# Performance work log

Measured on AMD Instinct MI355X. Metric: run time of the kernel, lower is better.

## Reference

```python
import jax, jax.numpy as jnp
import numpy as np

B, S, H, E, V, L = 64, 400, 512, 300, 50000, 1


def setup_inputs() -> dict:
    key = jax.random.key(0)
    ks = jax.random.split(key, 16)
    s = lambda k, shape, fan: jax.random.normal(k, shape, jnp.float32) * (1.0 / np.sqrt(fan))
    return {
        "x": jax.random.randint(ks[0], (B,), 0, V),
        "enc_out": jax.random.normal(ks[1], (B, S, H), jnp.float32),
        "h0": jax.random.normal(ks[2], (L, B, H), jnp.float32),
        "c0": jax.random.normal(ks[3], (L, B, H), jnp.float32),
        "text": jax.random.randint(ks[4], (B, S), 0, V),
        "batch_size": B,
        "emb_table": jax.random.normal(ks[5], (V, E), jnp.float32),
        "V_w": s(ks[6], (1, H), H),
        "V_b": jnp.zeros((1,), jnp.float32),
        "gen_w": s(ks[7], (1, 2 * H + E), 2 * H + E),
        "gen_b": jnp.zeros((1,), jnp.float32),
        "out_w": s(ks[8], (V, 2 * H), 2 * H),
        "out_b": jnp.zeros((V,), jnp.float32),
        "W_ih": s(ks[9], (4 * H, E + H), E + H),
        "W_hh": s(ks[10], (4 * H, H), H),
        "b_ih": jnp.zeros((4 * H,), jnp.float32),
        "b_hh": jnp.zeros((4 * H,), jnp.float32),
    }


def reference(x, enc_out, h0, c0, text, batch_size, emb_table, V_w, V_b,
              gen_w, gen_b, out_w, out_b, W_ih, W_hh, b_ih, b_hh):
    xe = emb_table[x]                                   # [B,E] (dropout off in eval)
    h_prev, c_prev = h0[0], c0[0]                       # [B,H], layers==1
    # Bahdanau attention: V(tanh(enc_out + dec_h)) softmaxed over seq
    score = jnp.tanh(enc_out + h_prev[:, None, :]) @ V_w.T + V_b   # [B,S,1]
    enc_weight = jax.nn.softmax(score, axis=1)                      # [B,S,1]
    ctx = jnp.sum(enc_weight * enc_out, axis=1)                     # [B,H]
    # single-step LSTM cell (torch gate order: i,f,g,o)
    d_in = jnp.concatenate([xe, ctx], axis=-1)                      # [B,E+H]
    gates = d_in @ W_ih.T + h_prev @ W_hh.T + b_ih + b_hh           # [B,4H]
    i, f, g, o = jnp.split(gates, 4, axis=-1)
    c_new = jax.nn.sigmoid(f) * c_prev + jax.nn.sigmoid(i) * jnp.tanh(g)
    h_new = jax.nn.sigmoid(o) * jnp.tanh(c_new)                     # [B,H]
    # pointer-generator combine
    out_cat = jnp.concatenate([h_new, ctx], axis=-1)                # [B,2H]
    gen_in = jnp.concatenate([ctx, h_new, xe], axis=-1)             # [B,2H+E]
    p_gen = jax.nn.sigmoid(gen_in @ gen_w.T + gen_b)[:, 0]          # [B]
    p_ptr = 1.0 - p_gen
    rows = jnp.arange(batch_size)[:, None]                          # [B,1]
    ptr_prob = jnp.zeros((batch_size, out_w.shape[0]), enc_out.dtype)
    ptr_prob = ptr_prob.at[rows, text].set(enc_weight[:, :, 0])     # scatter-set
    gen_prob = out_cat @ out_w.T + out_b                            # [B,V]
    out_prob = p_ptr[:, None] * ptr_prob + p_gen[:, None] * gen_prob
    return out_prob, h_new[None], c_new[None]
```

## Files before the change

kernel.cpp:

```cpp
#include <hip/hip_runtime.h>
#include <hip/hip_bf16.h>

#define BB 64
#define SS 400
#define HH 512
#define EE 300
#define VV 50000
#define KD 812
#define KG 1324
#define KC 1024
#define BV (BB*VV)

typedef __attribute__((ext_vector_type(8))) short bf16x8;
typedef __attribute__((ext_vector_type(4))) float f32x4;
typedef __attribute__((address_space(1))) const void gv_t;
typedef __attribute__((address_space(3))) void lv_t;

#define WS_SCORE 0
#define WS_W     25600
#define WS_CTX   51200
#define WS_HNEW  83968
#define WS_G0    116736
#define WS_G1    247808
#define WS_G2    378880
#define WS_G3    509952
#define WS_PGEN  641024
#define WS_PART  641088
#define WS_ABF   903232
#define WS_AD1   936000
#define WS_AD2   962624

__device__ __forceinline__ float sigm(float x){ return 1.f/(1.f+__expf(-x)); }
__device__ __forceinline__ float ftanh(float x){
  x = fminf(fmaxf(x,-15.f),15.f);
  float e = __expf(2.f*x);
  return (e-1.f)/(e+1.f);
}
__device__ __forceinline__ unsigned short f2bf(float f){
  unsigned int u = __builtin_bit_cast(unsigned int, f);
  u += 0x7fffu + ((u>>16)&1u);
  return (unsigned short)(u>>16);
}

#define LDW(S, off) { w##S##0 = *(const float4*)(wr + (off)*32); \
                      w##S##1 = *(const float4*)(wr + (off)*32 + 4); }
#define LDA(S, off) { a##S##0 = *(const bf16x8*)(a0 + (off)*32); \
                      a##S##1 = *(const bf16x8*)(a1 + (off)*32); \
                      a##S##2 = *(const bf16x8*)(a2 + (off)*32); \
                      a##S##3 = *(const bf16x8*)(a3 + (off)*32); }
#define CONS(S) { union { bf16x8 v; unsigned int u[4]; } bb_; \
  float4 f0_ = w##S##0; float4 f1_ = w##S##1; \
  asm("v_cvt_pk_bf16_f32 %0, %1, %2" : "=v"(bb_.u[0]) : "v"(f0_.x), "v"(f0_.y)); \
  asm("v_cvt_pk_bf16_f32 %0, %1, %2" : "=v"(bb_.u[1]) : "v"(f0_.z), "v"(f0_.w)); \
  asm("v_cvt_pk_bf16_f32 %0, %1, %2" : "=v"(bb_.u[2]) : "v"(f1_.x), "v"(f1_.y)); \
  asm("v_cvt_pk_bf16_f32 %0, %1, %2" : "=v"(bb_.u[3]) : "v"(f1_.z), "v"(f1_.w)); \
  acc0 = __builtin_amdgcn_mfma_f32_16x16x32_bf16(a##S##0, bb_.v, acc0, 0,0,0); \
  acc1 = __builtin_amdgcn_mfma_f32_16x16x32_bf16(a##S##1, bb_.v, acc1, 0,0,0); \
  acc2 = __builtin_amdgcn_mfma_f32_16x16x32_bf16(a##S##2, bb_.v, acc2, 0,0,0); \
  acc3 = __builtin_amdgcn_mfma_f32_16x16x32_bf16(a##S##3, bb_.v, acc3, 0,0,0); }

template<int NSTEP>
__device__ __forceinline__ void mfma_seg2(const float* __restrict__ wr,
    const unsigned short* __restrict__ a0, const unsigned short* __restrict__ a1,
    const unsigned short* __restrict__ a2, const unsigned short* __restrict__ a3,
    f32x4& acc0, f32x4& acc1, f32x4& acc2, f32x4& acc3)
{
  static_assert(NSTEP % 2 == 0 && NSTEP >= 4, "");
  float4 wA0,wA1, wB0,wB1;
  bf16x8 aA0,aA1,aA2,aA3, aB0,aB1,aB2,aB3;
  LDW(A,0) LDA(A,0)
  LDW(B,1) LDA(B,1)
  #pragma unroll
  for (int ks=0; ks<NSTEP; ks+=2){
    CONS(A) if (ks+2 < NSTEP){ LDW(A,ks+2) LDA(A,ks+2) }
    CONS(B) if (ks+3 < NSTEP){ LDW(B,ks+3) LDA(B,ks+3) }
  }
}

__global__ __launch_bounds__(256) void k_prep(const int* __restrict__ x,
    const float* __restrict__ emb, const float* __restrict__ h0,
    unsigned short* __restrict__ ad1, unsigned short* __restrict__ ad2)
{
  int n = blockIdx.x*256 + threadIdx.x;
  if (n < BB*832){
    int b = n/832, k = n - b*832;
    if (k < EE) ad1[n] = f2bf(emb[(size_t)x[b]*EE + k]);
    else if (k >= 812) ad1[n] = 0;
  } else {
    int m = n - BB*832;
    ad2[m] = f2bf(h0[m]);
  }
}

__global__ __launch_bounds__(256) void k_score(const float* __restrict__ enc,
    const float* __restrict__ h0, const float* __restrict__ Vw,
    const float* __restrict__ Vb, float* __restrict__ score)
{
  int wv = threadIdx.x >> 6, lane = threadIdx.x & 63;
  int pair = blockIdx.x*4 + wv;
  int b = pair / SS;
  int i0 = lane*8;
  const float4* ep = (const float4*)(enc + (size_t)pair*HH + i0);
  const float4* hp = (const float4*)(h0 + b*HH + i0);
  const float4* vp = (const float4*)(Vw + i0);
  float4 e0 = ep[0], e1 = ep[1];
  float4 hv0 = hp[0], hv1 = hp[1];
  float4 v0 = vp[0], v1 = vp[1];
  float sum = ftanh(e0.x+hv0.x)*v0.x + ftanh(e0.y+hv0.y)*v0.y
            + ftanh(e0.z+hv0.z)*v0.z + ftanh(e0.w+hv0.w)*v0.w
            + ftanh(e1.x+hv1.x)*v1.x + ftanh(e1.y+hv1.y)*v1.y
            + ftanh(e1.z+hv1.z)*v1.z + ftanh(e1.w+hv1.w)*v1.w;
  #pragma unroll
  for (int off=32; off; off>>=1) sum += __shfl_xor(sum, off);
  if (lane==0) score[pair] = sum + Vb[0];
}

__global__ __launch_bounds__(256) void k_ctx(const float* __restrict__ enc,
    const float* __restrict__ score, float* __restrict__ wout,
    float* __restrict__ part)
{
  __shared__ float red[256];
  __shared__ float wl[SS];
  int b = blockIdx.x >> 3, sp = blockIdx.x & 7;
  int t = threadIdx.x;
  float v1 = score[b*SS + t];
  float v2 = (t < SS-256) ? score[b*SS + t + 256] : -1e30f;
  red[t] = fmaxf(v1, v2);
  __syncthreads();
  for (int o=128; o; o>>=1){ if (t<o) red[t] = fmaxf(red[t], red[t+o]); __syncthreads(); }
  float mx = red[0];
  __syncthreads();
  float e1 = __expf(v1 - mx);
  float e2 = (t < SS-256) ? __expf(v2 - mx) : 0.f;
  red[t] = e1 + e2;
  __syncthreads();
  for (int o=128; o; o>>=1){ if (t<o) red[t] += red[t+o]; __syncthreads(); }
  float inv = 1.f/red[0];
  float w1 = e1*inv;
  wl[t] = w1;
  if (sp==0) wout[b*SS + t] = w1;
  if (t < SS-256){
    float w2 = e2*inv;
    wl[t+256] = w2;
    if (sp==0) wout[b*SS + t + 256] = w2;
  }
  __syncthreads();
  float a0 = 0.f, a1 = 0.f;
  const float* ebase = enc + ((size_t)b*SS + sp*50)*HH + 2*t;
  #pragma unroll 5
  for (int s=0; s<50; ++s){
    float wg = wl[sp*50 + s];
    float2 e = *(const float2*)(ebase + s*HH);
    a0 += wg * e.x;
    a1 += wg * e.y;
  }
  *(float2*)(part + (size_t)(b*8+sp)*HH + 2*t) = make_float2(a0, a1);
}

__global__ __launch_bounds__(256) void k_ctx_reduce(const float* __restrict__ part,
    float* __restrict__ ctx, unsigned short* __restrict__ ad1)
{
  int b = blockIdx.x, t = threadIdx.x;
  float a0=0.f, a1=0.f;
  #pragma unroll
  for (int sp=0; sp<8; ++sp){
    float2 e = *(const float2*)(part + (size_t)(b*8+sp)*HH + 2*t);
    a0 += e.x; a1 += e.y;
  }
  *(float2*)(ctx + b*HH + 2*t) = make_float2(a0, a1);
  ad1[b*832 + EE + 2*t]     = f2bf(a0);
  ad1[b*832 + EE + 2*t + 1] = f2bf(a1);
}

__global__ __launch_bounds__(128, 4) void k_gates(const float* __restrict__ Wih,
    const float* __restrict__ Whh, const unsigned short* __restrict__ ad1,
    const unsigned short* __restrict__ ad2,
    float* __restrict__ g0, float* __restrict__ g1,
    float* __restrict__ g2, float* __restrict__ g3)
{
  int wt = blockIdx.x*2 + (threadIdx.x >> 6);
  int lane = threadIdx.x & 63;
  int col = lane & 15, kg = lane >> 4;
  int jt = wt >> 2, part = wt & 3;
  int j = jt*16 + col;
  f32x4 acc0={0.f,0.f,0.f,0.f}, acc1=acc0, acc2=acc0, acc3=acc0;
  float* g;
  if (part < 2){
    int k0 = part ? 384 : 0;
    const float* wr = Wih + (size_t)j*KD + k0 + kg*8;
    const unsigned short* a = ad1 + col*832 + k0 + kg*8;
    if (part) mfma_seg2<14>(wr, a, a+16*832, a+32*832, a+48*832, acc0,acc1,acc2,acc3);
    else      mfma_seg2<12>(wr, a, a+16*832, a+32*832, a+48*832, acc0,acc1,acc2,acc3);
    g = part ? g1 : g0;
  } else {
    int k0 = (part==3) ? 256 : 0;
    const float* wr = Whh + (size_t)j*HH + k0 + kg*8;
    const unsigned short* a = ad2 + col*512 + k0 + kg*8;
    mfma_seg2<8>(wr, a, a+16*512, a+32*512, a+48*512, acc0,acc1,acc2,acc3);
    g = (part==3) ? g3 : g2;
  }
  #pragma unroll
  for (int i=0;i<4;i++){
    g[(size_t)j*BB + 0*16 + kg*4 + i] = acc0[i];
    g[(size_t)j*BB + 1*16 + kg*4 + i] = acc1[i];
    g[(size_t)j*BB + 2*16 + kg*4 + i] = acc2[i];
    g[(size_t)j*BB + 3*16 + kg*4 + i] = acc3[i];
  }
}

__global__ __launch_bounds__(256) void k_lstm(const float* __restrict__ c0,
    const float* __restrict__ bih, const float* __restrict__ bhh,
    const float* __restrict__ g0, const float* __restrict__ g1,
    const float* __restrict__ g2, const float* __restrict__ g3,
    const float* __restrict__ ctx, float* __restrict__ hnew,
    unsigned short* __restrict__ abf, float* __restrict__ out)
{
  int n = blockIdx.x*256 + threadIdx.x;
  int b = n & 63, h = n >> 6;
  #define GSUM(off) (g0[(off)*BB+b] + g1[(off)*BB+b] + g2[(off)*BB+b] + g3[(off)*BB+b] + bih[off] + bhh[off])
  float gi = GSUM(h);
  float gf = GSUM(HH+h);
  float gg = GSUM(2*HH+h);
  float go = GSUM(3*HH+h);
  #undef GSUM
  float cn = sigm(gf)*c0[b*HH+h] + sigm(gi)*ftanh(gg);
  float hn = sigm(go)*ftanh(cn);
  out[BV + b*HH + h]          = hn;
  out[BV + BB*HH + b*HH + h]  = cn;
  hnew[b*HH + h] = hn;
  abf[b*KC + h]      = f2bf(hn);
  abf[b*KC + HH + h] = f2bf(ctx[b*HH + h]);
}

__global__ __launch_bounds__(256) void k_pgen(const float* __restrict__ genw,
    const float* __restrict__ genb, const float* __restrict__ ctx,
    const float* __restrict__ hnew, const int* __restrict__ x,
    const float* __restrict__ emb, float* __restrict__ pgen)
{
  __shared__ float red[256];
  int b = blockIdx.x, t = threadIdx.x;
  float p = 0.f;
  for (int k=t; k<KG; k+=256){
    float g = genw[k];
    float v = (k < HH) ? ctx[b*HH + k]
            : (k < 2*HH) ? hnew[b*HH + k - HH]
            : emb[(size_t)x[b]*EE + (k - 2*HH)];
    p += g*v;
  }
  red[t] = p; __syncthreads();
  for (int o=128; o; o>>=1){ if (t<o) red[t] += red[t+o]; __syncthreads(); }
  if (t==0) pgen[b] = sigm(red[0] + genb[0]);
}

#define ROWB 4096
#define HROWB 2048
#define PADH 2064
__global__ __launch_bounds__(256, 2) void k_gemm(const float* __restrict__ out_w,
    const float* __restrict__ out_b, const unsigned short* __restrict__ abf,
    const float* __restrict__ pgen, float* __restrict__ out)
{
  __shared__ __align__(16) char wlds[2][16*PADH];
  int t = threadIdx.x;
  int w = t >> 6, lane = t & 63;
  int col = lane & 15, kg = lane >> 4;
  int bid = blockIdx.x;
  int ts = (bid * 3125) >> 9;
  int te = ((bid + 1) * 3125) >> 9;

  const unsigned short* ap = abf + (size_t)(w*16 + col)*KC + kg*8;
  bf16x8 pa0[16], pa1[16];
  #pragma unroll
  for (int ks=0; ks<16; ++ks){
    pa0[ks] = *(const bf16x8*)(ap + ks*32);
    pa1[ks] = *(const bf16x8*)(ap + 512 + ks*32);
  }

  #define DMASTEP(buf_, tile_, kh_) { \
    const char* wb_ = (const char*)out_w + (size_t)(tile_)*16*ROWB + (kh_)*HROWB; \
    _Pragma("unroll") \
    for (int i_=0;i_<8;i_++){ \
      int c_ = w*8 + i_; \
      int r_ = c_ >> 1, q_ = c_ & 1; \
      __builtin_amdgcn_global_load_lds( \
        (gv_t*)(wb_ + (size_t)r_*ROWB + q_*1024 + lane*16), \
        (lv_t*)(&wlds[buf_][0] + r_*PADH + q_*1024), 16, 0, 0); \
    } }

  #define HALFCOMPUTE(buf_, PA_) { \
    const char* rb_ = &wlds[buf_][0] + col*PADH + kg*32; \
    _Pragma("unroll") \
    for (int ks=0; ks<16; ++ks){ \
      float4 f0 = *(const float4*)(rb_ + ks*128); \
      float4 f1 = *(const float4*)(rb_ + ks*128 + 16); \
      union { bf16x8 v; unsigned int u[4]; } bb; \
      asm("v_cvt_pk_bf16_f32 %0, %1, %2" : "=v"(bb.u[0]) : "v"(f0.x), "v"(f0.y)); \
      asm("v_cvt_pk_bf16_f32 %0, %1, %2" : "=v"(bb.u[1]) : "v"(f0.z), "v"(f0.w)); \
      asm("v_cvt_pk_bf16_f32 %0, %1, %2" : "=v"(bb.u[2]) : "v"(f1.x), "v"(f1.y)); \
      asm("v_cvt_pk_bf16_f32 %0, %1, %2" : "=v"(bb.u[3]) : "v"(f1.z), "v"(f1.w)); \
      acc = __builtin_amdgcn_mfma_f32_16x16x32_bf16(PA_[ks], bb.v, acc, 0,0,0); \
    } }

  DMASTEP(0, ts, 0)
  int cur = 0;
  for (int tile = ts; tile < te; ++tile){
    f32x4 acc = {0.f,0.f,0.f,0.f};

    __syncthreads();
    DMASTEP(cur^1, tile, 1)
    HALFCOMPUTE(cur, pa0)
    cur ^= 1;

    __syncthreads();
    if (tile + 1 < te) DMASTEP(cur^1, tile+1, 0)
    HALFCOMPUTE(cur, pa1)
    cur ^= 1;

    int v = tile*16 + col;
    float ob = out_b[v];
    #pragma unroll
    for (int i=0;i<4;i++){
      int b = w*16 + kg*4 + i;
      out[(size_t)b*VV + v] = pgen[b]*(acc[i] + ob);
    }
  }
  #undef DMASTEP
  #undef HALFCOMPUTE
}

__global__ __launch_bounds__(256) void k_scatter(const int* __restrict__ text,
    const float* __restrict__ w, const float* __restrict__ pgen,
    float* __restrict__ out)
{
  __shared__ int ts[SS];
  int b = blockIdx.x, t = threadIdx.x;
  ts[t] = text[b*SS + t];
  if (t + 256 < SS) ts[t+256] = text[b*SS + t + 256];
  __syncthreads();
  float pp = 1.f - pgen[b];
  #pragma unroll
  for (int rep=0; rep<2; ++rep){
    int s = t + rep*256;
    if (s < SS){
      int v = ts[s];
      bool dup = false;
      #pragma unroll 4
      for (int s2=s+1; s2<SS; ++s2) dup = dup || (ts[s2]==v);
      if (!dup) out[(size_t)b*VV + v] += pp * w[b*SS + s];
    }
  }
}

extern "C" void kernel_launch(void* const* d_in, const int* in_sizes, int n_in,
                              void* d_out, int out_size, void* d_ws, size_t ws_size,
                              hipStream_t stream)
{
  const int*   x    = (const int*)  d_in[0];
  const float* enc  = (const float*)d_in[1];
  const float* h0   = (const float*)d_in[2];
  const float* c0   = (const float*)d_in[3];
  const int*   text = (const int*)  d_in[4];
  const float* emb  = (const float*)d_in[6];
  const float* Vw   = (const float*)d_in[7];
  const float* Vb   = (const float*)d_in[8];
  const float* genw = (const float*)d_in[9];
  const float* genb = (const float*)d_in[10];
  const float* outw = (const float*)d_in[11];
  const float* outb = (const float*)d_in[12];
  const float* Wih  = (const float*)d_in[13];
  const float* Whh  = (const float*)d_in[14];
  const float* bih  = (const float*)d_in[15];
  const float* bhh  = (const float*)d_in[16];
  float* out = (float*)d_out;

  float* ws     = (float*)d_ws;
  float* score  = ws + WS_SCORE;
  float* wbuf   = ws + WS_W;
  float* ctx    = ws + WS_CTX;
  float* hnew   = ws + WS_HNEW;
  float* g0     = ws + WS_G0;
  float* g1     = ws + WS_G1;
  float* g2     = ws + WS_G2;
  float* g3     = ws + WS_G3;
  float* pgen   = ws + WS_PGEN;
  float* part   = ws + WS_PART;
  unsigned short* abf = (unsigned short*)(ws + WS_ABF);
  unsigned short* ad1 = (unsigned short*)(ws + WS_AD1);
  unsigned short* ad2 = (unsigned short*)(ws + WS_AD2);

  k_prep<<<336, 256, 0, stream>>>(x, emb, h0, ad1, ad2);
  k_score<<<6400, 256, 0, stream>>>(enc, h0, Vw, Vb, score);
  k_ctx<<<512, 256, 0, stream>>>(enc, score, wbuf, part);
  k_ctx_reduce<<<64, 256, 0, stream>>>(part, ctx, ad1);
  k_gates<<<256, 128, 0, stream>>>(Wih, Whh, ad1, ad2, g0, g1, g2, g3);
  k_lstm<<<128, 256, 0, stream>>>(c0, bih, bhh, g0, g1, g2, g3, ctx, hnew, abf, out);
  k_pgen<<<64, 256, 0, stream>>>(genw, genb, ctx, hnew, x, emb, pgen);
  k_gemm<<<512, 256, 0, stream>>>(outw, outb, abf, pgen, out);
  k_scatter<<<64, 256, 0, stream>>>(text, wbuf, pgen, out);
}
```

Measured before the change: 126.1 us.

## Fuse score into ctx with split softmax; restage gemm weight loads via registers

The score and context kernels merge into one. Each block scores its own 50-position chunk, keeps a local max and sum, and writes unnormalised partial contexts that the reduce kernel rescales flash-style. The scatter kernel recomputes the normalised weights from the scores. Separately, the output GEMM drops direct global-to-LDS DMA in favour of register-staged quarter-K double buffering with manual waitcnt and barriers. This removes a launch and a second pass over enc_out, at the cost of different load scheduling and more barriers in the GEMM.

```diff
diff --git a/kernel.cpp b/kernel.cpp
--- a/kernel.cpp
+++ b/kernel.cpp
@@ -13,11 +13,10 @@
 
 typedef __attribute__((ext_vector_type(8))) short bf16x8;
 typedef __attribute__((ext_vector_type(4))) float f32x4;
-typedef __attribute__((address_space(1))) const void gv_t;
-typedef __attribute__((address_space(3))) void lv_t;
 
 #define WS_SCORE 0
-#define WS_W     25600
+#define WS_ML    25600
+#define WS_MLB   26624
 #define WS_CTX   51200
 #define WS_HNEW  83968
 #define WS_G0    116736
@@ -92,84 +91,79 @@
   }
 }
 
-__global__ __launch_bounds__(256) void k_score(const float* __restrict__ enc,
+__global__ __launch_bounds__(256) void k_scorectx(const float* __restrict__ enc,
     const float* __restrict__ h0, const float* __restrict__ Vw,
-    const float* __restrict__ Vb, float* __restrict__ score)
-{
-  int wv = threadIdx.x >> 6, lane = threadIdx.x & 63;
-  int pair = blockIdx.x*4 + wv;
-  int b = pair / SS;
+    const float* __restrict__ Vb, float* __restrict__ score,
+    float* __restrict__ part, float* __restrict__ ml)
+{
+  __shared__ float wl[52];
+  __shared__ float we[52];
+  int b = blockIdx.x >> 3, sp = blockIdx.x & 7;
+  int t = threadIdx.x, w = t >> 6, lane = t & 63;
   int i0 = lane*8;
-  const float4* ep = (const float4*)(enc + (size_t)pair*HH + i0);
   const float4* hp = (const float4*)(h0 + b*HH + i0);
   const float4* vp = (const float4*)(Vw + i0);
-  float4 e0 = ep[0], e1 = ep[1];
   float4 hv0 = hp[0], hv1 = hp[1];
   float4 v0 = vp[0], v1 = vp[1];
-  float sum = ftanh(e0.x+hv0.x)*v0.x + ftanh(e0.y+hv0.y)*v0.y
-            + ftanh(e0.z+hv0.z)*v0.z + ftanh(e0.w+hv0.w)*v0.w
-            + ftanh(e1.x+hv1.x)*v1.x + ftanh(e1.y+hv1.y)*v1.y
-            + ftanh(e1.z+hv1.z)*v1.z + ftanh(e1.w+hv1.w)*v1.w;
-  #pragma unroll
-  for (int off=32; off; off>>=1) sum += __shfl_xor(sum, off);
-  if (lane==0) score[pair] = sum + Vb[0];
-}
-
-__global__ __launch_bounds__(256) void k_ctx(const float* __restrict__ enc,
-    const float* __restrict__ score, float* __restrict__ wout,
-    float* __restrict__ part)
-{
-  __shared__ float red[256];
-  __shared__ float wl[SS];
-  int b = blockIdx.x >> 3, sp = blockIdx.x & 7;
-  int t = threadIdx.x;
-  float v1 = score[b*SS + t];
-  float v2 = (t < SS-256) ? score[b*SS + t + 256] : -1e30f;
-  red[t] = fmaxf(v1, v2);
+  float vb = Vb[0];
+  for (int r = w; r < 50; r += 4){
+    int s = sp*50 + r;
+    const float4* ep = (const float4*)(enc + ((size_t)b*SS + s)*HH + i0);
+    float4 e0 = ep[0], e1 = ep[1];
+    float sum = ftanh(e0.x+hv0.x)*v0.x + ftanh(e0.y+hv0.y)*v0.y
+              + ftanh(e0.z+hv0.z)*v0.z + ftanh(e0.w+hv0.w)*v0.w
+              + ftanh(e1.x+hv1.x)*v1.x + ftanh(e1.y+hv1.y)*v1.y
+              + ftanh(e1.z+hv1.z)*v1.z + ftanh(e1.w+hv1.w)*v1.w;
+    #pragma unroll
+    for (int off=32; off; off>>=1) sum += __shfl_xor(sum, off);
+    if (lane==0){ float sc = sum + vb; wl[r] = sc; score[b*SS + s] = sc; }
+  }
   __syncthreads();
-  for (int o=128; o; o>>=1){ if (t<o) red[t] = fmaxf(red[t], red[t+o]); __syncthreads(); }
-  float mx = red[0];
+  float mx = -1e30f;
+  for (int s=0; s<50; ++s) mx = fmaxf(mx, wl[s]);
+  if (t < 50) we[t] = __expf(wl[t] - mx);
   __syncthreads();
-  float e1 = __expf(v1 - mx);
-  float e2 = (t < SS-256) ? __expf(v2 - mx) : 0.f;
-  red[t] = e1 + e2;
-  __syncthreads();
-  for (int o=128; o; o>>=1){ if (t<o) red[t] += red[t+o]; __syncthreads(); }
-  float inv = 1.f/red[0];
-  float w1 = e1*inv;
-  wl[t] = w1;
-  if (sp==0) wout[b*SS + t] = w1;
-  if (t < SS-256){
-    float w2 = e2*inv;
-    wl[t+256] = w2;
-    if (sp==0) wout[b*SS + t + 256] = w2;
-  }
-  __syncthreads();
+  float l = 0.f;
+  for (int s=0; s<50; ++s) l += we[s];
   float a0 = 0.f, a1 = 0.f;
   const float* ebase = enc + ((size_t)b*SS + sp*50)*HH + 2*t;
   #pragma unroll 5
   for (int s=0; s<50; ++s){
-    float wg = wl[sp*50 + s];
+    float wg = we[s];
     float2 e = *(const float2*)(ebase + s*HH);
     a0 += wg * e.x;
     a1 += wg * e.y;
   }
   *(float2*)(part + (size_t)(b*8+sp)*HH + 2*t) = make_float2(a0, a1);
+  if (t == 0){ ml[(b*8+sp)*2] = mx; ml[(b*8+sp)*2+1] = l; }
 }
 
 __global__ __launch_bounds__(256) void k_ctx_reduce(const float* __restrict__ part,
-    float* __restrict__ ctx, unsigned short* __restrict__ ad1)
+    const float* __restrict__ ml, float* __restrict__ ctx,
+    unsigned short* __restrict__ ad1, float* __restrict__ mlb)
 {
   int b = blockIdx.x, t = threadIdx.x;
+  float M = -1e30f;
+  #pragma unroll
+  for (int c=0; c<8; ++c) M = fmaxf(M, ml[(b*8+c)*2]);
+  float L = 0.f, sc[8];
+  #pragma unroll
+  for (int c=0; c<8; ++c){
+    sc[c] = __expf(ml[(b*8+c)*2] - M);
+    L += ml[(b*8+c)*2+1] * sc[c];
+  }
+  float inv = 1.f / L;
   float a0=0.f, a1=0.f;
   #pragma unroll
-  for (int sp=0; sp<8; ++sp){
-    float2 e = *(const float2*)(part + (size_t)(b*8+sp)*HH + 2*t);
-    a0 += e.x; a1 += e.y;
-  }
+  for (int c=0; c<8; ++c){
+    float2 e = *(const float2*)(part + (size_t)(b*8+c)*HH + 2*t);
+    a0 += sc[c]*e.x; a1 += sc[c]*e.y;
+  }
+  a0 *= inv; a1 *= inv;
   *(float2*)(ctx + b*HH + 2*t) = make_float2(a0, a1);
   ad1[b*832 + EE + 2*t]     = f2bf(a0);
   ad1[b*832 + EE + 2*t + 1] = f2bf(a1);
+  if (t == 0){ mlb[b*2] = M; mlb[b*2+1] = L; }
 }
 
 __global__ __launch_bounds__(128, 4) void k_gates(const float* __restrict__ Wih,
@@ -252,44 +246,45 @@
   if (t==0) pgen[b] = sigm(red[0] + genb[0]);
 }
 
-#define ROWB 4096
-#define HROWB 2048
-#define PADH 2064
+#define QPAD 1040
 __global__ __launch_bounds__(256, 2) void k_gemm(const float* __restrict__ out_w,
     const float* __restrict__ out_b, const unsigned short* __restrict__ abf,
     const float* __restrict__ pgen, float* __restrict__ out)
 {
-  __shared__ __align__(16) char wlds[2][16*PADH];
-  int t = threadIdx.x;
-  int w = t >> 6, lane = t & 63;
+  __shared__ __align__(16) char wlds[2][16*QPAD];
+  int t = threadIdx.x, w = t >> 6, lane = t & 63;
   int col = lane & 15, kg = lane >> 4;
   int bid = blockIdx.x;
   int ts = (bid * 3125) >> 9;
   int te = ((bid + 1) * 3125) >> 9;
+  int NS = (te - ts) * 4;
 
   const unsigned short* ap = abf + (size_t)(w*16 + col)*KC + kg*8;
-  bf16x8 pa0[16], pa1[16];
-  #pragma unroll
-  for (int ks=0; ks<16; ++ks){
-    pa0[ks] = *(const bf16x8*)(ap + ks*32);
-    pa1[ks] = *(const bf16x8*)(ap + 512 + ks*32);
-  }
-
-  #define DMASTEP(buf_, tile_, kh_) { \
-    const char* wb_ = (const char*)out_w + (size_t)(tile_)*16*ROWB + (kh_)*HROWB; \
+  bf16x8 pa[32];
+  #pragma unroll
+  for (int k=0; k<32; ++k) pa[k] = *(const bf16x8*)(ap + k*32);
+
+  float4 st0, st1, st2, st3;
+  #define LOADSTEP(h_) { \
+    int tile_ = ts + ((h_) >> 2), q_ = (h_) & 3; \
+    const char* gp_ = (const char*)out_w + (size_t)tile_*65536 + (w*4)*4096 + q_*1024 + lane*16; \
+    st0 = *(const float4*)(gp_); \
+    st1 = *(const float4*)(gp_ + 4096); \
+    st2 = *(const float4*)(gp_ + 8192); \
+    st3 = *(const float4*)(gp_ + 12288); }
+  #define WRITESTEP(buf_) { \
+    char* lp_ = &wlds[buf_][0] + (w*4)*QPAD + lane*16; \
+    *(float4*)(lp_)          = st0; \
+    *(float4*)(lp_ + QPAD)   = st1; \
+    *(float4*)(lp_ + 2*QPAD) = st2; \
+    *(float4*)(lp_ + 3*QPAD) = st3; }
+  #define RAWBAR() { asm volatile("" ::: "memory"); \
+    __builtin_amdgcn_s_barrier(); \
+    asm volatile("" ::: "memory"); }
+  #define QCOMP(QL) { \
+    const char* rb_ = &wlds[h & 1][0] + col*QPAD + kg*32; \
     _Pragma("unroll") \
-    for (int i_=0;i_<8;i_++){ \
-      int c_ = w*8 + i_; \
-      int r_ = c_ >> 1, q_ = c_ & 1; \
-      __builtin_amdgcn_global_load_lds( \
-        (gv_t*)(wb_ + (size_t)r_*ROWB + q_*1024 + lane*16), \
-        (lv_t*)(&wlds[buf_][0] + r_*PADH + q_*1024), 16, 0, 0); \
-    } }
-
-  #define HALFCOMPUTE(buf_, PA_) { \
-    const char* rb_ = &wlds[buf_][0] + col*PADH + kg*32; \
-    _Pragma("unroll") \
-    for (int ks=0; ks<16; ++ks){ \
+    for (int ks=0; ks<8; ++ks){ \
       float4 f0 = *(const float4*)(rb_ + ks*128); \
       float4 f1 = *(const float4*)(rb_ + ks*128 + 16); \
       union { bf16x8 v; unsigned int u[4]; } bb; \
@@ -297,39 +292,54 @@
       asm("v_cvt_pk_bf16_f32 %0, %1, %2" : "=v"(bb.u[1]) : "v"(f0.z), "v"(f0.w)); \
       asm("v_cvt_pk_bf16_f32 %0, %1, %2" : "=v"(bb.u[2]) : "v"(f1.x), "v"(f1.y)); \
       asm("v_cvt_pk_bf16_f32 %0, %1, %2" : "=v"(bb.u[3]) : "v"(f1.z), "v"(f1.w)); \
-      acc = __builtin_amdgcn_mfma_f32_16x16x32_bf16(PA_[ks], bb.v, acc, 0,0,0); \
+      acc = __builtin_amdgcn_mfma_f32_16x16x32_bf16(pa[(QL)*8+ks], bb.v, acc, 0,0,0); \
     } }
 
-  DMASTEP(0, ts, 0)
-  int cur = 0;
-  for (int tile = ts; tile < te; ++tile){
-    f32x4 acc = {0.f,0.f,0.f,0.f};
-
-    __syncthreads();
-    DMASTEP(cur^1, tile, 1)
-    HALFCOMPUTE(cur, pa0)
-    cur ^= 1;
-
-    __syncthreads();
-    if (tile + 1 < te) DMASTEP(cur^1, tile+1, 0)
-    HALFCOMPUTE(cur, pa1)
-    cur ^= 1;
-
-    int v = tile*16 + col;
-    float ob = out_b[v];
-    #pragma unroll
-    for (int i=0;i<4;i++){
-      int b = w*16 + kg*4 + i;
-      out[(size_t)b*VV + v] = pgen[b]*(acc[i] + ob);
+  LOADSTEP(0)
+  asm volatile("s_waitcnt vmcnt(0)" ::: "memory");
+  __builtin_amdgcn_sched_barrier(0);
+  WRITESTEP(0)
+  asm volatile("s_waitcnt lgkmcnt(0)" ::: "memory");
+  RAWBAR();
+
+  f32x4 acc = {0.f,0.f,0.f,0.f};
+  for (int h = 0; h < NS; ++h){
+    int q = h & 3;
+    if (h + 1 < NS) LOADSTEP(h+1)
+
+    if      (q == 0){ QCOMP(0) }
+    else if (q == 1){ QCOMP(1) }
+    else if (q == 2){ QCOMP(2) }
+    else            { QCOMP(3) }
+
+    if (h + 1 < NS){
+      asm volatile("s_waitcnt vmcnt(0)" ::: "memory");
+      __builtin_amdgcn_sched_barrier(0);
+      WRITESTEP((h+1) & 1)
+      asm volatile("s_waitcnt lgkmcnt(0)" ::: "memory");
     }
-  }
-  #undef DMASTEP
-  #undef HALFCOMPUTE
+    if (q == 3){
+      int tile = ts + (h >> 2);
+      int v = tile*16 + col;
+      float ob = out_b[v];
+      #pragma unroll
+      for (int i=0;i<4;i++){
+        int b = w*16 + kg*4 + i;
+        out[(size_t)b*VV + v] = pgen[b]*(acc[i] + ob);
+      }
+      acc = (f32x4){0.f,0.f,0.f,0.f};
+    }
+    RAWBAR();
+  }
+  #undef LOADSTEP
+  #undef WRITESTEP
+  #undef RAWBAR
+  #undef QCOMP
 }
 
 __global__ __launch_bounds__(256) void k_scatter(const int* __restrict__ text,
-    const float* __restrict__ w, const float* __restrict__ pgen,
-    float* __restrict__ out)
+    const float* __restrict__ score, const float* __restrict__ mlb,
+    const float* __restrict__ pgen, float* __restrict__ out)
 {
   __shared__ int ts[SS];
   int b = blockIdx.x, t = threadIdx.x;
@@ -337,6 +347,7 @@
   if (t + 256 < SS) ts[t+256] = text[b*SS + t + 256];
   __syncthreads();
   float pp = 1.f - pgen[b];
+  float M = mlb[b*2], invL = 1.f / mlb[b*2+1];
   #pragma unroll
   for (int rep=0; rep<2; ++rep){
     int s = t + rep*256;
@@ -345,7 +356,10 @@
       bool dup = false;
       #pragma unroll 4
       for (int s2=s+1; s2<SS; ++s2) dup = dup || (ts[s2]==v);
-      if (!dup) out[(size_t)b*VV + v] += pp * w[b*SS + s];
+      if (!dup){
+        float wgt = __expf(score[b*SS + s] - M) * invL;
+        out[(size_t)b*VV + v] += pp * wgt;
+      }
     }
   }
 }
@@ -374,7 +388,8 @@
 
   float* ws     = (float*)d_ws;
   float* score  = ws + WS_SCORE;
-  float* wbuf   = ws + WS_W;
+  float* ml     = ws + WS_ML;
+  float* mlb    = ws + WS_MLB;
   float* ctx    = ws + WS_CTX;
   float* hnew   = ws + WS_HNEW;
   float* g0     = ws + WS_G0;
@@ -388,12 +403,11 @@
   unsigned short* ad2 = (unsigned short*)(ws + WS_AD2);
 
   k_prep<<<336, 256, 0, stream>>>(x, emb, h0, ad1, ad2);
-  k_score<<<6400, 256, 0, stream>>>(enc, h0, Vw, Vb, score);
-  k_ctx<<<512, 256, 0, stream>>>(enc, score, wbuf, part);
-  k_ctx_reduce<<<64, 256, 0, stream>>>(part, ctx, ad1);
+  k_scorectx<<<512, 256, 0, stream>>>(enc, h0, Vw, Vb, score, part, ml);
+  k_ctx_reduce<<<64, 256, 0, stream>>>(part, ml, ctx, ad1, mlb);
   k_gates<<<256, 128, 0, stream>>>(Wih, Whh, ad1, ad2, g0, g1, g2, g3);
   k_lstm<<<128, 256, 0, stream>>>(c0, bih, bhh, g0, g1, g2, g3, ctx, hnew, abf, out);
   k_pgen<<<64, 256, 0, stream>>>(genw, genb, ctx, hnew, x, emb, pgen);
   k_gemm<<<512, 256, 0, stream>>>(outw, outb, abf, pgen, out);
-  k_scatter<<<64, 256, 0, stream>>>(text, wbuf, pgen, out);
-}
+  k_scatter<<<64, 256, 0, stream>>>(text, score, mlb, pgen, out);
+}
```

New measurement: 126.5 us. About the same (+0.3%).
